# Optimization experiments

Hardware: AMD Instinct MI355X
Metric: run time of the kernel (lower is better)

## Reference

```python
import jax, jax.numpy as jnp
import numpy as np

N_HEADS = 32
N_KV_HEADS = 8
HEAD_DIM = 128
N_REP = N_HEADS // N_KV_HEADS
Q_SIZE = N_HEADS * HEAD_DIM        # 4096
K_SIZE = N_KV_HEADS * HEAD_DIM     # 1024


def setup_inputs() -> dict:
    key = jax.random.key(0)
    ks = jax.random.split(key, 5)
    B, T, D = 2, 2048, 4096
    x = jax.random.normal(ks[0], (B, T, D), dtype=jnp.float32)
    # complex freqs_cis split into real (cos) and imag (sin) parts, [T, head_dim/2]
    pos = jnp.arange(T, dtype=jnp.float32)[:, None]
    inv_freq = 1.0 / (10000.0 ** (jnp.arange(0, HEAD_DIM, 2, dtype=jnp.float32) / HEAD_DIM))
    ang = pos * inv_freq[None, :]
    freqs_cos = jnp.cos(ang)
    freqs_sin = jnp.sin(ang)
    w_qkv = jax.random.normal(ks[1], (Q_SIZE + 2 * K_SIZE, D), dtype=jnp.float32) * (D ** -0.5)
    wo_w = jax.random.normal(ks[2], (D, Q_SIZE), dtype=jnp.float32) * (Q_SIZE ** -0.5)
    return {"x": x, "freqs_cos": freqs_cos, "freqs_sin": freqs_sin, "w_qkv": w_qkv, "wo_w": wo_w}


def _apply_rotary(t, cos, sin):
    # t: [B, T, H, D]; cos/sin: [T, D/2] -> broadcast to [1, T, 1, D/2]
    tr = t.reshape(t.shape[:-1] + (HEAD_DIM // 2, 2))
    t0, t1 = tr[..., 0], tr[..., 1]
    c = cos[None, :, None, :]
    s = sin[None, :, None, :]
    o0 = t0 * c - t1 * s
    o1 = t0 * s + t1 * c
    return jnp.stack([o0, o1], axis=-1).reshape(t.shape)


def reference(x, freqs_cos, freqs_sin, w_qkv, wo_w):
    B, T, _ = x.shape
    qkv = jnp.einsum('btd,nd->btn', x, w_qkv)  # fused QKV GEMM
    q = qkv[..., :Q_SIZE].reshape(B, T, N_HEADS, HEAD_DIM)
    k = qkv[..., Q_SIZE:Q_SIZE + K_SIZE].reshape(B, T, N_KV_HEADS, HEAD_DIM)
    v = qkv[..., Q_SIZE + K_SIZE:].reshape(B, T, N_KV_HEADS, HEAD_DIM)
    q = _apply_rotary(q, freqs_cos, freqs_sin)
    k = _apply_rotary(k, freqs_cos, freqs_sin)
    # [B, H, T, D]
    q = q.transpose(0, 2, 1, 3)
    k = k.transpose(0, 2, 1, 3)
    v = v.transpose(0, 2, 1, 3)
    # GQA repeat_interleave along head dim
    k = jnp.repeat(k, N_REP, axis=1)
    v = jnp.repeat(v, N_REP, axis=1)
    scale = HEAD_DIM ** -0.5
    scores = jnp.einsum('bhqd,bhkd->bhqk', q, k) * scale
    causal = jnp.tril(jnp.ones((T, T), dtype=bool))
    scores = jnp.where(causal[None, None], scores, jnp.finfo(scores.dtype).min)
    attn = jax.nn.softmax(scores, axis=-1)
    y = jnp.einsum('bhqk,bhkd->bhqd', attn, v)
    y = y.transpose(0, 2, 1, 3).reshape(B, T, Q_SIZE)
    return jnp.einsum('btn,dn->btd', y, wo_w)
```

## Files before the change

kernel.cpp:

```cpp
#include <hip/hip_runtime.h>

typedef unsigned short u16t;
typedef unsigned int   u32t;
typedef __attribute__((ext_vector_type(8))) __bf16          bf16x8;
typedef __attribute__((ext_vector_type(8))) unsigned short  u16x8;
typedef __attribute__((ext_vector_type(4))) unsigned short  u16x4;
typedef __attribute__((ext_vector_type(4))) float           floatx4;

__device__ __forceinline__ u16t f2b(float f){
  u32t u = __builtin_bit_cast(u32t, f);
  u += 0x7fffu + ((u >> 16) & 1u);
  return (u16t)(u >> 16);
}
__device__ __forceinline__ float b2f(u16t h){
  return __builtin_bit_cast(float, (u32t)h << 16);
}
__device__ __forceinline__ void async16(const void* g, void* l){
  __builtin_amdgcn_global_load_lds((__attribute__((address_space(1))) void*)g,
                                   (__attribute__((address_space(3))) void*)l, 16, 0, 0);
}
__device__ __forceinline__ bf16x8 ldfrag(const u16t* p){
  return __builtin_bit_cast(bf16x8, *(const u16x8*)p);
}

__global__ __launch_bounds__(256)
void cvt_f32_bf16(const float* __restrict__ in, u16t* __restrict__ out, int n4){
  typedef __attribute__((ext_vector_type(4))) float f32x4;
  const f32x4* in4 = (const f32x4*)in;
  int stride = gridDim.x * blockDim.x;
  for (int i = blockIdx.x * blockDim.x + threadIdx.x; i < n4; i += stride){
    f32x4 v = in4[i];
    u16x4 o; o[0]=f2b(v[0]); o[1]=f2b(v[1]); o[2]=f2b(v[2]); o[3]=f2b(v[3]);
    *(u16x4*)(out + (size_t)i * 4) = o;
  }
}

#define MFMA16 __builtin_amdgcn_mfma_f32_16x16x32_bf16
template<int OUT_BF16>
__global__ __launch_bounds__(512, 2)
void gemm256(const u16t* __restrict__ A, const u16t* __restrict__ B,
             void* __restrict__ Cv, int M, int N, int K)
{
  (void)M;
  __shared__ u16t smem[65536];
  const int tid  = threadIdx.x;
  const int w    = tid >> 6, lane = tid & 63;
  const int lrow = lane & 15, quad = lane >> 4;
  const int wr   = w >> 2,  wc = w & 3;

  const int gm = (int)gridDim.y, gn = (int)gridDim.x;
  const int cm = gm >> 1, cn = gn >> 2;
  const int flat = (int)(blockIdx.y * gridDim.x + blockIdx.x);
  const int xcd = flat & 7, idx = flat >> 3;
  const int m0 = ((xcd & 1) * cm + (idx % cm)) * 256;
  const int n0 = ((xcd >> 1) * cn + (idx / cm)) * 256;

  const int srow = lane >> 3;
  const int scol = ((lane & 7) ^ srow) * 8;
  const u16t* gA = A + (size_t)(m0 + w * 8 + srow) * K + scol;
  const u16t* gB = B + (size_t)(n0 + w * 8 + srow) * K + scol;
  char* const ldsA = (char*)smem + w * 1024;
  char* const ldsB = (char*)smem + 65536 + w * 1024;
#define STA(h, i, buf, kt) async16(gA + (size_t)((h)*128 + (i)*64) * K + (kt)*64, \
                                   ldsA + (buf)*32768 + ((h)*2+(i))*8192)
#define STB(h, i, buf, kt) async16(gB + (size_t)((h)*128 + (i)*64) * K + (kt)*64, \
                                   ldsB + (buf)*32768 + ((h)*2+(i))*8192)

  const char* const sbb = (const char*)smem;
  const int c0   = ((quad ^ (lrow & 7)) * 16);
  const int aoff = (wr * 128 + lrow) * 128;
  const int boff = 65536 + (wc * 64 + lrow) * 128;

  floatx4 acc[8][4] = {};
  bf16x8 A0f[4][2], A1f[4][2], Bf0[2][2], Bf1[2][2];
  const int NT = K >> 6;

  STA(0,0,0,0); STA(0,1,0,0); STA(1,0,0,0); STA(1,1,0,0);
  STB(0,0,0,0); STB(0,1,0,0); STB(1,0,0,0); STB(1,1,0,0);
  STA(0,0,1,1); STA(0,1,1,1); STA(1,0,1,1); STA(1,1,1,1);
  STB(0,0,1,1); STB(0,1,1,1);
  asm volatile("s_waitcnt vmcnt(6)" ::: "memory");
  __builtin_amdgcn_sched_barrier(0);
  __builtin_amdgcn_s_barrier();

  for (int t = 0; t < NT; ++t){
    const int bsel = t & 1, nb = bsel ^ 1;
    const int bo = bsel * 32768;

#pragma unroll
    for (int mi = 0; mi < 4; ++mi){
      A0f[mi][0] = ldfrag((const u16t*)(sbb + bo + aoff + mi * 2048 + c0));
      A0f[mi][1] = ldfrag((const u16t*)(sbb + bo + aoff + mi * 2048 + (c0 ^ 64)));
    }
#pragma unroll
    for (int ni = 0; ni < 2; ++ni){
      Bf0[ni][0] = ldfrag((const u16t*)(sbb + bo + boff + ni * 2048 + c0));
      Bf0[ni][1] = ldfrag((const u16t*)(sbb + bo + boff + ni * 2048 + (c0 ^ 64)));
    }
    if (t + 1 < NT){ STB(1,0,nb,t+1); STB(1,1,nb,t+1); }
    __builtin_amdgcn_s_barrier();
    asm volatile("s_waitcnt lgkmcnt(0)" ::: "memory");
    __builtin_amdgcn_sched_barrier(0);
    __builtin_amdgcn_s_setprio(1);
#pragma unroll
    for (int mi = 0; mi < 4; ++mi)
#pragma unroll
      for (int ni = 0; ni < 2; ++ni){
        acc[mi][ni] = MFMA16(A0f[mi][0], Bf0[ni][0], acc[mi][ni], 0, 0, 0);
        acc[mi][ni] = MFMA16(A0f[mi][1], Bf0[ni][1], acc[mi][ni], 0, 0, 0);
      }
    __builtin_amdgcn_s_setprio(0);
    __builtin_amdgcn_sched_barrier(0);
    __builtin_amdgcn_s_barrier();

#pragma unroll
    for (int mi = 0; mi < 4; ++mi){
      A1f[mi][0] = ldfrag((const u16t*)(sbb + bo + aoff + (4 + mi) * 2048 + c0));
      A1f[mi][1] = ldfrag((const u16t*)(sbb + bo + aoff + (4 + mi) * 2048 + (c0 ^ 64)));
    }
    if (t + 2 < NT){ STA(0,0,bsel,t+2); STA(0,1,bsel,t+2); }
    __builtin_amdgcn_s_barrier();
    asm volatile("s_waitcnt lgkmcnt(8)" ::: "memory");
    __builtin_amdgcn_sched_barrier(0);
    __builtin_amdgcn_s_setprio(1);
#pragma unroll
    for (int mi = 0; mi < 4; ++mi)
#pragma unroll
      for (int ni = 0; ni < 2; ++ni){
        acc[4+mi][ni] = MFMA16(A1f[mi][0], Bf0[ni][0], acc[4+mi][ni], 0, 0, 0);
        acc[4+mi][ni] = MFMA16(A1f[mi][1], Bf0[ni][1], acc[4+mi][ni], 0, 0, 0);
      }
    __builtin_amdgcn_s_setprio(0);
    __builtin_amdgcn_sched_barrier(0);
    __builtin_amdgcn_s_barrier();

#pragma unroll
    for (int ni = 0; ni < 2; ++ni){
      Bf1[ni][0] = ldfrag((const u16t*)(sbb + bo + boff + (2 + ni) * 2048 + c0));
      Bf1[ni][1] = ldfrag((const u16t*)(sbb + bo + boff + (2 + ni) * 2048 + (c0 ^ 64)));
    }
    if (t + 2 < NT){ STA(1,0,bsel,t+2); STA(1,1,bsel,t+2); }
    __builtin_amdgcn_s_barrier();
    asm volatile("s_waitcnt lgkmcnt(4)" ::: "memory");
    __builtin_amdgcn_sched_barrier(0);
    __builtin_amdgcn_s_setprio(1);
#pragma unroll
    for (int mi = 0; mi < 4; ++mi)
#pragma unroll
      for (int ni = 0; ni < 2; ++ni){
        acc[mi][2+ni] = MFMA16(A0f[mi][0], Bf1[ni][0], acc[mi][2+ni], 0, 0, 0);
        acc[mi][2+ni] = MFMA16(A0f[mi][1], Bf1[ni][1], acc[mi][2+ni], 0, 0, 0);
      }
    __builtin_amdgcn_s_setprio(0);
    __builtin_amdgcn_sched_barrier(0);
    __builtin_amdgcn_s_barrier();

    if (t + 2 < NT){ STB(0,0,bsel,t+2); STB(0,1,bsel,t+2); }
    __builtin_amdgcn_s_barrier();
    asm volatile("s_waitcnt lgkmcnt(0)" ::: "memory");
    __builtin_amdgcn_sched_barrier(0);
    __builtin_amdgcn_s_setprio(1);
#pragma unroll
    for (int mi = 0; mi < 4; ++mi)
#pragma unroll
      for (int ni = 0; ni < 2; ++ni){
        acc[4+mi][2+ni] = MFMA16(A1f[mi][0], Bf1[ni][0], acc[4+mi][2+ni], 0, 0, 0);
        acc[4+mi][2+ni] = MFMA16(A1f[mi][1], Bf1[ni][1], acc[4+mi][2+ni], 0, 0, 0);
      }
    __builtin_amdgcn_s_setprio(0);
    __builtin_amdgcn_sched_barrier(0);
    if (t + 2 < NT) asm volatile("s_waitcnt vmcnt(6)" ::: "memory");
    else            asm volatile("s_waitcnt vmcnt(0)" ::: "memory");
    __builtin_amdgcn_sched_barrier(0);
    __builtin_amdgcn_s_barrier();
  }

#pragma unroll
  for (int mi = 0; mi < 8; ++mi)
#pragma unroll
    for (int ni = 0; ni < 4; ++ni)
#pragma unroll
      for (int r = 0; r < 4; ++r){
        int row = m0 + wr * 128 + mi * 16 + quad * 4 + r;
        int col = n0 + wc * 64 + ni * 16 + lrow;
        float v = acc[mi][ni][r];
        if (OUT_BF16) ((u16t*)Cv)[(size_t)row * N + col] = f2b(v);
        else          ((float*)Cv)[(size_t)row * N + col] = v;
      }
#undef STA
#undef STB
}

__global__ __launch_bounds__(256)
void rope_qk(const u16t* __restrict__ qkvb, const float* __restrict__ cosp,
             const float* __restrict__ sinp, u16t* __restrict__ qr, u16t* __restrict__ kr)
{
  const int row = blockIdx.x;
  const int b = row >> 11, t = row & 2047;
  const u16t* src = qkvb + (size_t)row * 6144;
  for (int p = threadIdx.x; p < 2560; p += 256){
    u32t both = *(const u32t*)(src + 2 * p);
    float t0 = b2f((u16t)(both & 0xffff));
    float t1 = b2f((u16t)(both >> 16));
    int j = p & 63;
    float c = cosp[t * 64 + j], s = sinp[t * 64 + j];
    float o0 = t0 * c - t1 * s;
    float o1 = t0 * s + t1 * c;
    u32t packed = (u32t)f2b(o0) | ((u32t)f2b(o1) << 16);
    if (p < 2048){
      int h = p >> 6;
      *(u32t*)(qr + (((size_t)(b * 32 + h) * 2048 + t) * 128 + 2 * j)) = packed;
    } else {
      int kh = (p - 2048) >> 6;
      *(u32t*)(kr + (((size_t)(b * 8 + kh) * 2048 + t) * 128 + 2 * j)) = packed;
    }
  }
}

__global__ __launch_bounds__(256)
void vtrans(const u16t* __restrict__ qkvb, u16t* __restrict__ vt)
{
  __shared__ u16t sV[64 * 128];
  const int tid = threadIdx.x;
  const int blk = blockIdx.x;
  const int tile = blk & 31, kvh = (blk >> 5) & 7, b = blk >> 8;
  const int t0 = tile * 64;
  const size_t srcbase = (size_t)(b * 2048 + t0) * 6144 + 5120 + kvh * 128;
#pragma unroll
  for (int it = 0; it < 4; ++it){
    int task = it * 256 + tid;
    int rrow = task >> 4, cb = task & 15;
    *(u16x8*)&sV[rrow * 128 + cb * 8] =
        *(const u16x8*)(qkvb + srcbase + (size_t)rrow * 6144 + cb * 8);
  }
  __syncthreads();
  const size_t dstbase = (size_t)((b * 8 + kvh) * 128) * 2048 + t0;
#pragma unroll
  for (int it = 0; it < 4; ++it){
    int task = it * 256 + tid;
    int tc = task & 7, d = task >> 3;
    u16x8 v;
#pragma unroll
    for (int j = 0; j < 8; ++j) v[j] = sV[(tc * 8 + j) * 128 + d];
    *(u16x8*)(vt + dstbase + (size_t)d * 2048 + tc * 8) = v;
  }
}

__global__ __launch_bounds__(256)
void attn_fwd(const u16t* __restrict__ Qg, const u16t* __restrict__ Kg,
              const u16t* __restrict__ Vt, u16t* __restrict__ Y)
{
  __shared__ u16t smem[32768];
  u16t* sQ = smem;
  u16t* sP = smem;
  u16t* sK = smem + 16384;
  u16t* sV = smem + 24576;

  const int tid  = threadIdx.x;
  const int wave = tid >> 6, lane = tid & 63;
  const int lrow = lane & 15, quad = lane >> 4;
  const int qt = 15 - (int)blockIdx.y;
  const int q0 = qt * 128;
  const int bh = blockIdx.x;
  const int b = bh >> 5, h = bh & 31, kvh = h >> 2;
  const float qscale = 0.088388347648318447f * 1.4426950408889634f;

  const size_t qbase = ((size_t)bh * 2048 + q0) * 128;
#pragma unroll
  for (int r = 0; r < 8; ++r){
    const int c = wave * 8 + r;
    const int dc = c >> 1, half = c & 1;
    async16(Qg + qbase + (size_t)(half * 64 + lane) * 128 + dc * 8, (char*)sQ + c * 1024);
  }

  float mi[2][4], li[2][4];
#pragma unroll
  for (int qs = 0; qs < 2; ++qs)
#pragma unroll
    for (int r = 0; r < 4; ++r){ mi[qs][r] = -1e30f; li[qs][r] = 0.f; }
  floatx4 o[2][8] = {};
  bf16x8 aq[2][4];
  const size_t kbase = ((size_t)(b * 8 + kvh) * 2048) * 128;
  const size_t vbase = ((size_t)(b * 8 + kvh) * 128) * 2048;
  const int ktiles = 2 * qt + 2;

  for (int kt = 0; kt < ktiles; ++kt){
    const int k0 = kt * 64;
#pragma unroll
    for (int r = 0; r < 4; ++r){
      const int dc = r * 4 + wave;
      async16(Kg + kbase + (size_t)(k0 + lane) * 128 + dc * 8, (char*)sK + dc * 1024);
    }
#pragma unroll
    for (int r = 0; r < 4; ++r){
      const int kvc = r * 2 + (wave >> 1);
      const int dd  = (wave & 1) * 64 + lane;
      async16(Vt + vbase + (size_t)dd * 2048 + k0 + kvc * 8,
              (char*)sV + kvc * 2048 + (wave & 1) * 1024);
    }
    __syncthreads();

    if (kt == 0){
#pragma unroll
      for (int qs = 0; qs < 2; ++qs)
#pragma unroll
        for (int kk = 0; kk < 4; ++kk)
          aq[qs][kk] = ldfrag(&sQ[((kk * 4 + quad) * 128 + wave * 32 + qs * 16 + lrow) * 8]);
    }

    floatx4 s[2][4] = {};
#pragma unroll
    for (int kk = 0; kk < 4; ++kk){
#pragma unroll
      for (int nt = 0; nt < 4; ++nt){
        bf16x8 bk = ldfrag(&sK[((kk * 4 + quad) * 64 + nt * 16 + lrow) * 8]);
        s[0][nt] = __builtin_amdgcn_mfma_f32_16x16x32_bf16(aq[0][kk], bk, s[0][nt], 0, 0, 0);
        s[1][nt] = __builtin_amdgcn_mfma_f32_16x16x32_bf16(aq[1][kk], bk, s[1][nt], 0, 0, 0);
      }
    }
    if (kt == 0) __syncthreads();

#pragma unroll
    for (int qs = 0; qs < 2; ++qs){
      float tt[4][4];
#pragma unroll
      for (int nt = 0; nt < 4; ++nt)
#pragma unroll
        for (int r = 0; r < 4; ++r)
          tt[nt][r] = s[qs][nt][r] * qscale;
      const int qrb = q0 + wave * 32 + qs * 16 + quad * 4;
      if (kt >= ktiles - 2){
#pragma unroll
        for (int nt = 0; nt < 4; ++nt){
          int kc = k0 + nt * 16 + lrow;
#pragma unroll
          for (int r = 0; r < 4; ++r)
            if (kc > qrb + r) tt[nt][r] = -1e30f;
        }
      }
      float rmax[4];
#pragma unroll
      for (int r = 0; r < 4; ++r)
        rmax[r] = fmaxf(fmaxf(tt[0][r], tt[1][r]), fmaxf(tt[2][r], tt[3][r]));
#pragma unroll
      for (int off = 1; off < 16; off <<= 1){
#pragma unroll
        for (int r = 0; r < 4; ++r)
          rmax[r] = fmaxf(rmax[r], __shfl_xor(rmax[r], off, 64));
      }
      float alpha[4];
#pragma unroll
      for (int r = 0; r < 4; ++r){
        float mn = fmaxf(mi[qs][r], rmax[r]);
        alpha[r] = __builtin_amdgcn_exp2f(mi[qs][r] - mn);
        mi[qs][r] = mn;
      }
      float lsum[4] = {0.f, 0.f, 0.f, 0.f};
#pragma unroll
      for (int nt = 0; nt < 4; ++nt)
#pragma unroll
        for (int r = 0; r < 4; ++r){
          float e = __builtin_amdgcn_exp2f(tt[nt][r] - mi[qs][r]);
          lsum[r] += e;
          sP[(wave * 32 + qs * 16 + quad * 4 + r) * 72 + nt * 16 + lrow] = f2b(e);
        }
#pragma unroll
      for (int off = 1; off < 16; off <<= 1){
#pragma unroll
        for (int r = 0; r < 4; ++r)
          lsum[r] += __shfl_xor(lsum[r], off, 64);
      }
#pragma unroll
      for (int r = 0; r < 4; ++r) li[qs][r] = li[qs][r] * alpha[r] + lsum[r];
#pragma unroll
      for (int nt = 0; nt < 8; ++nt){
        o[qs][nt][0] *= alpha[0]; o[qs][nt][1] *= alpha[1];
        o[qs][nt][2] *= alpha[2]; o[qs][nt][3] *= alpha[3];
      }
    }

#pragma unroll
    for (int kk = 0; kk < 2; ++kk){
      bf16x8 ap0 = ldfrag(&sP[(wave * 32 + lrow) * 72 + kk * 32 + quad * 8]);
      bf16x8 ap1 = ldfrag(&sP[(wave * 32 + 16 + lrow) * 72 + kk * 32 + quad * 8]);
#pragma unroll
      for (int nt = 0; nt < 8; ++nt){
        bf16x8 bv = ldfrag(&sV[((kk * 4 + quad) * 128 + nt * 16 + lrow) * 8]);
        o[0][nt] = __builtin_amdgcn_mfma_f32_16x16x32_bf16(ap0, bv, o[0][nt], 0, 0, 0);
        o[1][nt] = __builtin_amdgcn_mfma_f32_16x16x32_bf16(ap1, bv, o[1][nt], 0, 0, 0);
      }
    }
    __syncthreads();
  }

#pragma unroll
  for (int qs = 0; qs < 2; ++qs)
#pragma unroll
    for (int r = 0; r < 4; ++r){
      int t = q0 + wave * 32 + qs * 16 + quad * 4 + r;
      float inv = 1.0f / li[qs][r];
      size_t ybase = ((size_t)(b * 2048 + t)) * 4096 + h * 128;
#pragma unroll
      for (int nt = 0; nt < 8; ++nt)
        Y[ybase + nt * 16 + lrow] = f2b(o[qs][nt][r] * inv);
    }
}

extern "C" void kernel_launch(void* const* d_in, const int* in_sizes, int n_in,
                              void* d_out, int out_size, void* d_ws, size_t ws_size,
                              hipStream_t stream)
{
  (void)in_sizes; (void)n_in; (void)out_size; (void)ws_size;
  const float* x    = (const float*)d_in[0];
  const float* fc   = (const float*)d_in[1];
  const float* fs   = (const float*)d_in[2];
  const float* wqkv = (const float*)d_in[3];
  const float* wo   = (const float*)d_in[4];
  float* out = (float*)d_out;

  char* ws = (char*)d_ws;
  u16t* xb    = (u16t*)(ws);
  u16t* wqkvb = (u16t*)(ws + 33554432);
  u16t* wob   = (u16t*)(ws + 83886080);
  u16t* qkvb  = (u16t*)(ws + 117440512);
  u16t* qr    = (u16t*)(ws + 167772160);
  u16t* kr    = (u16t*)(ws + 201326592);
  u16t* vt    = (u16t*)(ws + 209715200);
  u16t* yb    = xb;

  cvt_f32_bf16<<<4096, 256, 0, stream>>>(x,    xb,    16777216 / 4);
  cvt_f32_bf16<<<4096, 256, 0, stream>>>(wqkv, wqkvb, 25165824 / 4);
  cvt_f32_bf16<<<4096, 256, 0, stream>>>(wo,   wob,   16777216 / 4);
  gemm256<1><<<dim3(24, 16), 512, 0, stream>>>(xb, wqkvb, qkvb, 4096, 6144, 4096);
  rope_qk<<<4096, 256, 0, stream>>>(qkvb, fc, fs, qr, kr);
  vtrans<<<512, 256, 0, stream>>>(qkvb, vt);
  attn_fwd<<<dim3(64, 16), 256, 0, stream>>>(qr, kr, vt, yb);
  gemm256<0><<<dim3(16, 16), 512, 0, stream>>>(yb, wob, out, 4096, 4096, 4096);
}
```

Measured before the change: 869.7 us.

## Remap GEMM tile order, simplify LDS waits, load Q fragments directly in attention

The GEMM block-to-tile mapping changes from a 2x4 XCD-partitioned layout to a contiguous chunk-per-XCD ordering in row-major tile space, which alters L2 locality. The partial lgkmcnt waits become full waits, and one wait is dropped, simplifying the LDS synchronization schedule. The attention kernel loads Q fragments straight from global memory into registers instead of staging them in LDS, which shrinks shared memory and removes one block barrier. Full waits can expose more LDS latency, and the dropped wait could be a correctness risk if the later MFMAs depend on pending Bf1 loads.

Result: no change. 884.7 us (+1.7%).

```diff
diff --git a/kernel.cpp b/kernel.cpp
--- a/kernel.cpp
+++ b/kernel.cpp
@@ -48,12 +48,12 @@
   const int lrow = lane & 15, quad = lane >> 4;
   const int wr   = w >> 2,  wc = w & 3;
 
-  const int gm = (int)gridDim.y, gn = (int)gridDim.x;
-  const int cm = gm >> 1, cn = gn >> 2;
+  const int nwg  = (int)(gridDim.x * gridDim.y);
   const int flat = (int)(blockIdx.y * gridDim.x + blockIdx.x);
-  const int xcd = flat & 7, idx = flat >> 3;
-  const int m0 = ((xcd & 1) * cm + (idx % cm)) * 256;
-  const int n0 = ((xcd >> 1) * cn + (idx / cm)) * 256;
+  const int q8 = nwg >> 3, r8 = nwg & 7, xcd = flat & 7, idx = flat >> 3;
+  const int wg = (xcd < r8 ? xcd * (q8 + 1) : r8 * (q8 + 1) + (xcd - r8) * q8) + idx;
+  const int m0 = (wg / (int)gridDim.x) * 256;
+  const int n0 = (wg % (int)gridDim.x) * 256;
 
   const int srow = lane >> 3;
   const int scol = ((lane & 7) ^ srow) * 8;
@@ -120,7 +120,7 @@
     }
     if (t + 2 < NT){ STA(0,0,bsel,t+2); STA(0,1,bsel,t+2); }
     __builtin_amdgcn_s_barrier();
-    asm volatile("s_waitcnt lgkmcnt(8)" ::: "memory");
+    asm volatile("s_waitcnt lgkmcnt(0)" ::: "memory");
     __builtin_amdgcn_sched_barrier(0);
     __builtin_amdgcn_s_setprio(1);
 #pragma unroll
@@ -141,7 +141,7 @@
     }
     if (t + 2 < NT){ STA(1,0,bsel,t+2); STA(1,1,bsel,t+2); }
     __builtin_amdgcn_s_barrier();
-    asm volatile("s_waitcnt lgkmcnt(4)" ::: "memory");
+    asm volatile("s_waitcnt lgkmcnt(0)" ::: "memory");
     __builtin_amdgcn_sched_barrier(0);
     __builtin_amdgcn_s_setprio(1);
 #pragma unroll
@@ -157,8 +157,6 @@
 
     if (t + 2 < NT){ STB(0,0,bsel,t+2); STB(0,1,bsel,t+2); }
     __builtin_amdgcn_s_barrier();
-    asm volatile("s_waitcnt lgkmcnt(0)" ::: "memory");
-    __builtin_amdgcn_sched_barrier(0);
     __builtin_amdgcn_s_setprio(1);
 #pragma unroll
     for (int mi = 0; mi < 4; ++mi)
@@ -250,11 +248,10 @@
 void attn_fwd(const u16t* __restrict__ Qg, const u16t* __restrict__ Kg,
               const u16t* __restrict__ Vt, u16t* __restrict__ Y)
 {
-  __shared__ u16t smem[32768];
-  u16t* sQ = smem;
-  u16t* sP = smem;
-  u16t* sK = smem + 16384;
-  u16t* sV = smem + 24576;
+  __shared__ u16t smem[25600];
+  u16t* sK = smem;
+  u16t* sV = smem + 8192;
+  u16t* sP = smem + 16384;
 
   const int tid  = threadIdx.x;
   const int wave = tid >> 6, lane = tid & 63;
@@ -265,13 +262,13 @@
   const int b = bh >> 5, h = bh & 31, kvh = h >> 2;
   const float qscale = 0.088388347648318447f * 1.4426950408889634f;
 
-  const size_t qbase = ((size_t)bh * 2048 + q0) * 128;
-#pragma unroll
-  for (int r = 0; r < 8; ++r){
-    const int c = wave * 8 + r;
-    const int dc = c >> 1, half = c & 1;
-    async16(Qg + qbase + (size_t)(half * 64 + lane) * 128 + dc * 8, (char*)sQ + c * 1024);
-  }
+  bf16x8 aq[2][4];
+  const size_t qbase = ((size_t)bh * 2048 + q0 + wave * 32) * 128;
+#pragma unroll
+  for (int qs = 0; qs < 2; ++qs)
+#pragma unroll
+    for (int kk = 0; kk < 4; ++kk)
+      aq[qs][kk] = ldfrag(Qg + qbase + (size_t)(qs * 16 + lrow) * 128 + (kk * 4 + quad) * 8);
 
   float mi[2][4], li[2][4];
 #pragma unroll
@@ -279,7 +276,6 @@
 #pragma unroll
     for (int r = 0; r < 4; ++r){ mi[qs][r] = -1e30f; li[qs][r] = 0.f; }
   floatx4 o[2][8] = {};
-  bf16x8 aq[2][4];
   const size_t kbase = ((size_t)(b * 8 + kvh) * 2048) * 128;
   const size_t vbase = ((size_t)(b * 8 + kvh) * 128) * 2048;
   const int ktiles = 2 * qt + 2;
@@ -300,14 +296,6 @@
     }
     __syncthreads();
 
-    if (kt == 0){
-#pragma unroll
-      for (int qs = 0; qs < 2; ++qs)
-#pragma unroll
-        for (int kk = 0; kk < 4; ++kk)
-          aq[qs][kk] = ldfrag(&sQ[((kk * 4 + quad) * 128 + wave * 32 + qs * 16 + lrow) * 8]);
-    }
-
     floatx4 s[2][4] = {};
 #pragma unroll
     for (int kk = 0; kk < 4; ++kk){
@@ -318,7 +306,6 @@
         s[1][nt] = __builtin_amdgcn_mfma_f32_16x16x32_bf16(aq[1][kk], bk, s[1][nt], 0, 0, 0);
       }
     }
-    if (kt == 0) __syncthreads();
 
 #pragma unroll
     for (int qs = 0; qs < 2; ++qs){
```
